# Kernel optimization log

Hardware: AMD Instinct MI355X
Metric: run time of the kernel (lower is better)

Reference implementation:

```python
import jax, jax.numpy as jnp
import numpy as np

DILATIONS = (1, 3, 6, 12)          # layer dilations, flattened from [[1,3],[6,12]]
BLOCKS = ((0, 1), (2, 3))           # block -> layer indices
H_SIZE = 32
STATE_SIZE = 128
OUT_SIZE = STATE_SIZE - H_SIZE      # 96
INPUT_SIZE = 64
OUTPUT_SIZE = 64
T, B = 512, 512


def _linear_params(k, fan_in, fan_out):
    bound = 1.0 / np.sqrt(fan_in)
    kw, kb = jax.random.split(k)
    W = jax.random.uniform(kw, (fan_out, fan_in), minval=-bound, maxval=bound, dtype=jnp.float32)
    b = jax.random.uniform(kb, (fan_out,), minval=-bound, maxval=bound, dtype=jnp.float32)
    return W, b


def setup_inputs() -> dict:
    key = jax.random.key(0)
    ks = jax.random.split(key, 8)
    x = jax.random.normal(ks[0], (T, B, INPUT_SIZE), dtype=jnp.float32)
    ins = [INPUT_SIZE, OUT_SIZE, OUT_SIZE, OUT_SIZE]  # first layer sees raw input
    out = {"x": x}
    for l in range(4):
        W, b = _linear_params(ks[1 + l], ins[l] + 2 * H_SIZE, 4 * STATE_SIZE)
        out[f"W{l}"] = W
        out[f"b{l}"] = b
    Wa, ba = _linear_params(ks[5], OUT_SIZE, OUTPUT_SIZE)
    out["Wa"] = Wa
    out["ba"] = ba
    return out


def _s2cell(W, b, inp, prev_h, second_h, prev_c, delayed_c, has_prev, has_del):
    # xh = cat(input, prev_h, delayed_h-or-prev_h) ; zeros when no prev state (handled by caller masks)
    xh = jnp.concatenate([inp, prev_h, second_h], axis=1)
    g = xh @ W.T + b                                     # [B, 4*state]
    g0, g1, g2, g3 = jnp.split(g, 4, axis=1)
    forget = jax.nn.sigmoid(g0 + 1.0)
    cand = jnp.tanh(g1)
    alpha = jax.nn.sigmoid(g2)
    out_gate = jax.nn.sigmoid(g3)
    weighted = jnp.where(has_del, alpha * prev_c + (1.0 - alpha) * delayed_c, prev_c)
    new_c = jnp.where(has_prev, forget * weighted + (1.0 - forget) * cand, cand)
    whole = out_gate * new_c
    return whole[:, :OUT_SIZE], whole[:, OUT_SIZE:], new_c


def reference(x, W0, b0, W1, b1, W2, b2, W3, b3, Wa, ba):
    Ws = [W0, W1, W2, W3]
    bs = [b0, b1, b2, b3]
    batch = x.shape[1]
    h0 = tuple(jnp.zeros((d, batch, H_SIZE), jnp.float32) for d in DILATIONS)
    c0 = tuple(jnp.zeros((d, batch, STATE_SIZE), jnp.float32) for d in DILATIONS)

    def step(carry, inp_t):
        t, h_bufs, c_bufs = carry
        h_bufs = list(h_bufs)
        c_bufs = list(c_bufs)
        has_prev = t >= 1
        prev_block = None
        out_t = None
        for iblock, layers in enumerate(BLOCKS):
            for j, l in enumerate(layers):
                cur_in = (inp_t if iblock == 0 else prev_block) if j == 0 else out_t
                d = DILATIONS[l]
                # ring buffer: slot (t-1)%d holds state at t-1, slot t%d still holds state at t-d
                prev_h = jnp.where(has_prev, h_bufs[l][(t - 1) % d], 0.0)
                prev_c = c_bufs[l][(t - 1) % d]
                has_del = t >= d
                del_h = jnp.where(has_del, h_bufs[l][t % d], prev_h)
                del_c = c_bufs[l][t % d]
                out_t, new_h, new_c = _s2cell(Ws[l], bs[l], cur_in, prev_h, del_h,
                                              prev_c, del_c, has_prev, has_del)
                h_bufs[l] = h_bufs[l].at[t % d].set(new_h)
                c_bufs[l] = c_bufs[l].at[t % d].set(new_c)
            prev_block = out_t if iblock == 0 else out_t + prev_block  # resnet shortcut
        y = prev_block @ Wa.T + ba
        return (t + 1, tuple(h_bufs), tuple(c_bufs)), y

    _, ys = jax.lax.scan(step, (jnp.int32(0), h0, c0), x)
    return ys  # [T, B, output_size]
```

## Files before the change

### kernel.cpp

```cpp
#include <hip/hip_runtime.h>

typedef unsigned int uint;
typedef unsigned short ushort;
typedef unsigned long long u64;
typedef __attribute__((ext_vector_type(8))) short bf16x8;
typedef __attribute__((ext_vector_type(4))) float f32x4;

#define T_STEPS 512
#define BATCH   512
#define NB      8
#define XS      168
#define CSTR    12
#define OUTC    96
#define FSTR    32

__device__ __forceinline__ ushort f2bf(float f){
  uint u = __builtin_bit_cast(uint, f);
  u = (u + 0x7FFFu + ((u >> 16) & 1u)) >> 16;
  return (ushort)u;
}
__device__ __forceinline__ float bf2f(ushort h){
  uint u = ((uint)h) << 16; return __builtin_bit_cast(float, u);
}
__device__ __forceinline__ float sigm(float x){
  float e = __builtin_exp2f(-1.44269504f * x);
  return __builtin_amdgcn_rcpf(1.0f + e);
}
__device__ __forceinline__ float tanh_fast(float x){
  float e = __builtin_exp2f(-2.88539008f * x);
  return 2.0f * __builtin_amdgcn_rcpf(1.0f + e) - 1.0f;
}
__device__ __forceinline__ uint aload32(const uint* p){
  return __hip_atomic_load(p, __ATOMIC_RELAXED, __HIP_MEMORY_SCOPE_AGENT);
}
__device__ __forceinline__ void astore32(uint* p, uint v){
  __hip_atomic_store(p, v, __ATOMIC_RELAXED, __HIP_MEMORY_SCOPE_AGENT);
}
__device__ __forceinline__ u64 aload64(const u64* p){
  return __hip_atomic_load(p, __ATOMIC_RELAXED, __HIP_MEMORY_SCOPE_AGENT);
}
__device__ __forceinline__ void astore64(u64* p, u64 v){
  __hip_atomic_store(p, v, __ATOMIC_RELAXED, __HIP_MEMORY_SCOPE_AGENT);
}

__global__ __launch_bounds__(512, 1)
void rnn_pipeline(const float* __restrict__ x,
                  const float* __restrict__ W0, const float* __restrict__ b0,
                  const float* __restrict__ W1, const float* __restrict__ b1,
                  const float* __restrict__ W2, const float* __restrict__ b2,
                  const float* __restrict__ W3, const float* __restrict__ b3,
                  const float* __restrict__ Wa, const float* __restrict__ ba,
                  float* __restrict__ y_out,
                  uint* __restrict__ prod, uint* __restrict__ consA,
                  uint* __restrict__ consB,
                  u64* __restrict__ hop0, u64* __restrict__ hop1,
                  u64* __restrict__ hop2, int rd)
{
  const int tid  = threadIdx.x;
  const int wv   = tid >> 6;
  const int lane = tid & 63;
  const int l15  = lane & 15;
  const int hi   = lane >> 4;
  const int rep  = blockIdx.x & 63;
  const int stage= blockIdx.x >> 6;
  const int b0r  = rep * NB;
  const int rmask= rd - 1;

  const int dil = (stage==0)?1:(stage==1)?3:(stage==2)?6:12;
  const int KIN = (stage==0)?64:96;
  const int K   = KIN + 64;
  const float* Wl = (stage==0)?W0:(stage==1)?W1:(stage==2)?W2:W3;
  const float* bl = (stage==0)?b0:(stage==1)?b1:(stage==2)?b2:b3;

  __shared__ __align__(16) ushort xh_hi[16*XS], xh_lo[16*XS];
  __shared__ __align__(16) float  sh_c[12*128*CSTR];
  __shared__ __align__(16) ushort h_hi[12*NB*32], h_lo[12*NB*32];
  __shared__ __align__(16) ushort outp[2304];
  __shared__ __align__(16) ushort o1p[1536];
  __shared__ __align__(16) float  o3f[NB*OUTC];
  __shared__ __align__(16) float  yst[512];

  for (int i = tid; i < 16*XS; i += 512){ xh_hi[i] = 0; xh_lo[i] = 0; }
  for (int i = tid; i < 12*128*CSTR; i += 512) sh_c[i] = 0.0f;
  for (int i = tid; i < 12*NB*32; i += 512){ h_hi[i] = 0; h_lo[i] = 0; }
  for (int i = tid; i < 2304; i += 512) outp[i] = 0;
  for (int i = tid; i < 1536; i += 512) o1p[i] = 0;
  for (int i = tid; i < NB*OUTC; i += 512) o3f[i] = 0.0f;
  yst[tid] = 0.0f;

  const int sidx = 16*wv + l15;

  bf16x8 whi[4][5], wlo[4][5];
  #pragma unroll
  for (int j = 0; j < 4; ++j){
    const int grow = 128*j + sidx;
    #pragma unroll
    for (int ks = 0; ks < 5; ++ks){
      bf16x8 vh, vl;
      const int cb = ks*32 + hi*8;
      if (cb < K){
        const float* p = Wl + (size_t)grow*K + cb;
        #pragma unroll
        for (int i = 0; i < 8; ++i){
          float w = p[i];
          ushort h = f2bf(w);
          vh[i] = (short)h;
          vl[i] = (short)f2bf(w - bf2f(h));
        }
      } else {
        #pragma unroll
        for (int i = 0; i < 8; ++i){ vh[i] = 0; vl[i] = 0; }
      }
      whi[j][ks] = vh; wlo[j][ks] = vl;
    }
  }
  float bias[4];
  #pragma unroll
  for (int j = 0; j < 4; ++j) bias[j] = bl[128*j + sidx];

  bf16x8 phi[3], plo[3];
  #pragma unroll
  for (int ks = 0; ks < 3; ++ks){
    bf16x8 z;
    #pragma unroll
    for (int i = 0; i < 8; ++i) z[i]=0;
    phi[ks]=z; plo[ks]=z;
  }
  float bav = 0.0f;
  if (stage == 3 && wv < 4){
    const int ocol = 16*wv + l15;
    #pragma unroll
    for (int ks = 0; ks < 3; ++ks){
      const float* p = Wa + (size_t)ocol*96 + ks*32 + hi*8;
      bf16x8 vh, vl;
      #pragma unroll
      for (int i = 0; i < 8; ++i){
        float w = p[i];
        ushort h = f2bf(w);
        vh[i] = (short)h;
        vl[i] = (short)f2bf(w - bf2f(h));
      }
      phi[ks] = vh; plo[ks] = vl;
    }
    bav = ba[ocol];
  }

  uint* up_prod  = (stage==1)? &prod[rep*FSTR] : (stage==2)? &prod[(64+rep)*FSTR] :
                   (stage==3)? &prod[(128+rep)*FSTR] : nullptr;
  uint* up_prod1 = (stage==3)? &prod[(64+rep)*FSTR] : nullptr;
  uint* my_prod  = (stage==0)? &prod[rep*FSTR] : (stage==1)? &prod[(64+rep)*FSTR] :
                   (stage==2)? &prod[(128+rep)*FSTR] : nullptr;
  uint* my_consA = (stage==1)? &consA[rep*FSTR] : (stage==2)? &consA[(64+rep)*FSTR] :
                   (stage==3)? &consA[(128+rep)*FSTR] : nullptr;
  uint* my_consB = (stage==3)? &consB[rep*FSTR] : nullptr;
  uint* dnA      = (stage==0)? &consA[rep*FSTR] : (stage==1)? &consA[(64+rep)*FSTR] :
                   (stage==2)? &consA[(128+rep)*FSTR] : nullptr;
  uint* dnB      = (stage==1)? &consB[rep*FSTR] : nullptr;
  const u64* hop_in  = (stage==1)? hop0 : (stage==2)? hop1 : nullptr;
  u64*       hop_out = (stage==0)? hop0 : (stage==1)? hop1 : (stage==2)? hop2 : nullptr;

  __syncthreads();

  u64 pfA = 0, pfB = 0; float xv = 0.0f;
  uint fvU = 0, fvU1 = 0, fvDA = 0, fvDB = 0;
  if (stage == 0){
    xv = x[(size_t)(b0r + (tid>>6))*64 + (tid&63)];
  } else if (stage < 3){
    uint f = aload32(up_prod);
    while (f < 1u){ __builtin_amdgcn_s_sleep(2); f = aload32(up_prod); }
    if (tid < 384) pfA = aload64(hop_in + (size_t)rep*384 + tid);
  } else {
    uint f = aload32(up_prod);
    while (f < 1u){ __builtin_amdgcn_s_sleep(2); f = aload32(up_prod); }
    f = aload32(up_prod1);
    while (f < 1u){ __builtin_amdgcn_s_sleep(2); f = aload32(up_prod1); }
    const u64* s2 = hop2 + (size_t)rep*384;
    const u64* s1 = hop1 + (size_t)rep*384;
    pfA = (tid < 384) ? aload64(s2 + tid) : aload64(s1 + (tid - 384));
    if (tid < 256) pfB = aload64(s1 + 128 + tid);
  }

  int cur = 0, prv = dil - 1;
  for (int t = 0; t < T_STEPS; ++t){
    const int slot = t & rmask;

    asm volatile("s_waitcnt vmcnt(0)" ::: "memory");
    if (stage == 0){
      const int r = tid >> 6, c = tid & 63;
      ushort hb = f2bf(xv);
      xh_hi[r*XS + c] = hb;
      xh_lo[r*XS + c] = f2bf(xv - bf2f(hb));
    } else {
      if (tid < 384){
        const int q = (tid < 192) ? tid : tid - 192;
        ushort* plane = (tid < 192) ? xh_hi : xh_lo;
        const int r = q / 24, c4 = (q % 24) * 4;
        *(u64*)(plane + r*XS + c4) = pfA;
      } else if (stage == 3){
        *(u64*)(o1p + 4*(tid - 384)) = pfA;
      }
      if (stage == 3 && tid < 256) *(u64*)(o1p + 4*(128 + tid)) = pfB;
    }
    {
      const int which = tid >> 8, rem = tid & 255, r = rem >> 5, c = rem & 31;
      const int srcslot = (which == 1 && t >= dil) ? cur : prv;
      xh_hi[r*XS + KIN + which*32 + c] = h_hi[srcslot*(NB*32) + r*32 + c];
      xh_lo[r*XS + KIN + which*32 + c] = h_lo[srcslot*(NB*32) + r*32 + c];
    }
    __syncthreads();
    if (tid == 0){
      if (stage > 0){
        astore32(my_consA, (uint)(t+1));
        if (stage == 3) astore32(my_consB, (uint)(t+1));
      }
      if (stage < 3 && t >= 1) astore32(my_prod, (uint)t);
    }
    if (stage == 3 && t > 0){
      y_out[(size_t)((t-1)*BATCH + b0r + (tid>>6))*64 + (tid&63)] = yst[tid];
    }
    const bool pre = (t + 1 < T_STEPS);
    uint up_f = 0, up_f1 = 0;
    if (pre && stage > 0)  up_f  = aload32(up_prod);
    if (pre && stage == 3) up_f1 = aload32(up_prod1);
    if (stage < 3 && t >= rd)  fvDA = aload32(dnA);
    if (stage == 1 && t >= rd) fvDB = aload32(dnB);

    f32x4 acc[4];
    #pragma unroll
    for (int j = 0; j < 4; ++j) acc[j] = (f32x4){bias[j],bias[j],bias[j],bias[j]};
    const int abase = l15*XS + hi*8;
    #pragma unroll
    for (int ks = 0; ks < 5; ++ks){
      if (ks*32 < K){
        bf16x8 ahi = *(const bf16x8*)(xh_hi + abase + ks*32);
        bf16x8 alo = *(const bf16x8*)(xh_lo + abase + ks*32);
        #pragma unroll
        for (int j = 0; j < 4; ++j){
          acc[j] = __builtin_amdgcn_mfma_f32_16x16x32_bf16(ahi, whi[j][ks], acc[j], 0, 0, 0);
          acc[j] = __builtin_amdgcn_mfma_f32_16x16x32_bf16(alo, whi[j][ks], acc[j], 0, 0, 0);
          acc[j] = __builtin_amdgcn_mfma_f32_16x16x32_bf16(ahi, wlo[j][ks], acc[j], 0, 0, 0);
        }
      }
    }

    if (pre){
      if (stage == 0){
        xv = x[(size_t)((t+1)*BATCH + b0r + (tid>>6))*64 + (tid&63)];
      } else {
        const uint need = (uint)(t + 2);
        while (up_f < need){ __builtin_amdgcn_s_sleep(2); up_f = aload32(up_prod); }
        if (stage == 3)
          while (up_f1 < need){ __builtin_amdgcn_s_sleep(2); up_f1 = aload32(up_prod1); }
        const int ns = (t + 1) & rmask;
        if (stage < 3){
          if (tid < 384) pfA = aload64(hop_in + (size_t)(ns*64 + rep)*384 + tid);
        } else {
          const u64* s2 = hop2 + (size_t)(ns*64 + rep)*384;
          const u64* s1 = hop1 + (size_t)(ns*64 + rep)*384;
          pfA = (tid < 384) ? aload64(s2 + tid) : aload64(s1 + (tid - 384));
          if (tid < 256) pfB = aload64(s1 + 128 + tid);
        }
      }
    }

    f32x4 pc = *(const f32x4*)(sh_c + prv*(128*CSTR) + sidx*CSTR + (hi&1)*4);
    f32x4 dc = *(const f32x4*)(sh_c + cur*(128*CSTR) + sidx*CSTR + (hi&1)*4);
    const bool has_prev = (t >= 1), has_del = (t >= dil);
    f32x4 ncv; float whv[4];
    #pragma unroll
    for (int k = 0; k < 4; ++k){
      float f  = sigm(acc[0][k] + 1.0f);
      float cd = tanh_fast(acc[1][k]);
      float al = sigm(acc[2][k]);
      float og = sigm(acc[3][k]);
      float wt = has_del ? (al*pc[k] + (1.0f - al)*dc[k]) : pc[k];
      float nc = has_prev ? (f*wt + (1.0f - f)*cd) : cd;
      ncv[k] = nc;
      whv[k] = og * nc;
    }
    if (hi < 2){
      *(f32x4*)(sh_c + cur*(128*CSTR) + sidx*CSTR + hi*4) = ncv;
      #pragma unroll
      for (int k = 0; k < 4; ++k){
        const int r = hi*4 + k;
        const float w = whv[k];
        if (sidx < OUTC){
          if (stage == 3){
            o3f[r*OUTC + sidx] = w;
          } else {
            ushort hb = f2bf(w);
            outp[r*OUTC + sidx]       = hb;
            outp[768 + r*OUTC + sidx] = f2bf(w - bf2f(hb));
          }
        } else {
          ushort hb = f2bf(w);
          h_hi[cur*(NB*32) + r*32 + (sidx - OUTC)] = hb;
          h_lo[cur*(NB*32) + r*32 + (sidx - OUTC)] = f2bf(w - bf2f(hb));
        }
      }
    }
    __syncthreads();

    if (stage < 3){
      if (t >= rd){
        const uint need = (uint)(t - rd + 1);
        while (fvDA < need){ __builtin_amdgcn_s_sleep(2); fvDA = aload32(dnA); }
        if (stage == 1)
          while (fvDB < need){ __builtin_amdgcn_s_sleep(2); fvDB = aload32(dnB); }
      }
      if (tid < 384){
        u64 v = *(const u64*)(outp + 4*tid);
        astore64(hop_out + (size_t)(slot*64 + rep)*384 + tid, v);
      }
    } else {
      for (int j = tid; j < 768; j += 512){
        float v = o3f[j] + bf2f(o1p[j]) + bf2f(o1p[768 + j]);
        ushort hb = f2bf(v);
        outp[j]       = hb;
        outp[768 + j] = f2bf(v - bf2f(hb));
      }
      __syncthreads();
      if (wv < 4){
        f32x4 acc1 = (f32x4){bav, bav, bav, bav};
        const int pbase = l15*96 + hi*8;
        #pragma unroll
        for (int ks = 0; ks < 3; ++ks){
          bf16x8 ahi = *(const bf16x8*)(outp + pbase + ks*32);
          bf16x8 alo = *(const bf16x8*)(outp + 768 + pbase + ks*32);
          acc1 = __builtin_amdgcn_mfma_f32_16x16x32_bf16(ahi, phi[ks], acc1, 0, 0, 0);
          acc1 = __builtin_amdgcn_mfma_f32_16x16x32_bf16(alo, phi[ks], acc1, 0, 0, 0);
          acc1 = __builtin_amdgcn_mfma_f32_16x16x32_bf16(ahi, plo[ks], acc1, 0, 0, 0);
        }
        if (hi < 2){
          const int ocol = 16*wv + l15;
          #pragma unroll
          for (int k = 0; k < 4; ++k){
            yst[(hi*4 + k)*64 + ocol] = acc1[k];
          }
        }
      }
    }
    prv = cur;
    cur = (cur + 1 == dil) ? 0 : cur + 1;
  }

  asm volatile("s_waitcnt vmcnt(0)" ::: "memory");
  __syncthreads();
  if (stage == 3){
    y_out[(size_t)((T_STEPS-1)*BATCH + b0r + (tid>>6))*64 + (tid&63)] = yst[tid];
  }
  if (stage < 3 && tid == 0) astore32(my_prod, (uint)(T_STEPS + 2));
}

extern "C" void kernel_launch(void* const* d_in, const int* in_sizes, int n_in,
                              void* d_out, int out_size, void* d_ws, size_t ws_size,
                              hipStream_t stream) {
  (void)in_sizes; (void)n_in; (void)out_size;
  const float* x  = (const float*)d_in[0];
  const float* W0 = (const float*)d_in[1];
  const float* b0 = (const float*)d_in[2];
  const float* W1 = (const float*)d_in[3];
  const float* b1 = (const float*)d_in[4];
  const float* W2 = (const float*)d_in[5];
  const float* b2 = (const float*)d_in[6];
  const float* W3 = (const float*)d_in[7];
  const float* b3 = (const float*)d_in[8];
  const float* Wa = (const float*)d_in[9];
  const float* ba = (const float*)d_in[10];
  float* out = (float*)d_out;

  int rd = 16;
  if (ws_size > 65536){
    size_t avail = ws_size - 65536;
    while (rd < 512 && (size_t)(rd * 2) * 64 * 9216 <= avail) rd *= 2;
  }

  uint* prod  = (uint*)d_ws;
  uint* consA = (uint*)((char*)d_ws + 24576);
  uint* consB = (uint*)((char*)d_ws + 49152);
  u64* hop0 = (u64*)((char*)d_ws + 65536);
  u64* hop1 = hop0 + (size_t)rd*64*384;
  u64* hop2 = hop1 + (size_t)rd*64*384;

  hipMemsetAsync(d_ws, 0, 65536, stream);
  hipLaunchKernelGGL(rnn_pipeline, dim3(256), dim3(512), 0, stream,
                     x, W0, b0, W1, b1, W2, b2, W3, b3, Wa, ba,
                     out, prod, consA, consB, hop0, hop1, hop2, rd);
}
```

Measured before the change: 2.205 ms.

## Process two timesteps per iteration with double-buffered inter-stage handoff

Restructures the persistent pipelined recurrent kernel so each loop iteration handles two timesteps, with double-buffered shared input, output and residual buffers. The h/delayed-h operands are now read directly from a padded h ring buffer instead of being copied into the xh staging array. Flag polling is speculative, falling back to a lane-0 spin and refetch only when the prefetched flags are stale, and producer/consumer signals advance two steps at a time. The final projection is written straight to global memory. The goal is to halve barrier and handshake overhead per step and remove a copy, at the cost of more LDS, a doubled flag protocol whose correctness is subtle, and coarser inter-stage granularity.

```diff
diff --git a/kernel.cpp b/kernel.cpp
--- a/kernel.cpp
+++ b/kernel.cpp
@@ -9,10 +9,13 @@
 #define T_STEPS 512
 #define BATCH   512
 #define NB      8
-#define XS      168
+#define XS      104
+#define HS      40
+#define HSLOT   (16*HS)
 #define CSTR    12
 #define OUTC    96
 #define FSTR    32
+#define NITER   256
 
 __device__ __forceinline__ ushort f2bf(float f){
   uint u = __builtin_bit_cast(uint, f);
@@ -72,21 +75,20 @@
   const float* Wl = (stage==0)?W0:(stage==1)?W1:(stage==2)?W2:W3;
   const float* bl = (stage==0)?b0:(stage==1)?b1:(stage==2)?b2:b3;
 
-  __shared__ __align__(16) ushort xh_hi[16*XS], xh_lo[16*XS];
+  __shared__ __align__(16) ushort xiA_hi[16*XS], xiA_lo[16*XS];
+  __shared__ __align__(16) ushort xiB_hi[16*XS], xiB_lo[16*XS];
   __shared__ __align__(16) float  sh_c[12*128*CSTR];
-  __shared__ __align__(16) ushort h_hi[12*NB*32], h_lo[12*NB*32];
-  __shared__ __align__(16) ushort outp[2304];
-  __shared__ __align__(16) ushort o1p[1536];
-  __shared__ __align__(16) float  o3f[NB*OUTC];
-  __shared__ __align__(16) float  yst[512];
-
-  for (int i = tid; i < 16*XS; i += 512){ xh_hi[i] = 0; xh_lo[i] = 0; }
+  __shared__ __align__(16) ushort h_hi[12*HSLOT], h_lo[12*HSLOT];
+  __shared__ __align__(16) ushort outpA[2304], outpB[2304];
+  __shared__ __align__(16) ushort o1pA[1536], o1pB[1536];
+  __shared__ __align__(16) float  o3fA[768],  o3fB[768];
+
+  for (int i = tid; i < 16*XS; i += 512){ xiA_hi[i]=0; xiA_lo[i]=0; xiB_hi[i]=0; xiB_lo[i]=0; }
   for (int i = tid; i < 12*128*CSTR; i += 512) sh_c[i] = 0.0f;
-  for (int i = tid; i < 12*NB*32; i += 512){ h_hi[i] = 0; h_lo[i] = 0; }
-  for (int i = tid; i < 2304; i += 512) outp[i] = 0;
-  for (int i = tid; i < 1536; i += 512) o1p[i] = 0;
-  for (int i = tid; i < NB*OUTC; i += 512) o3f[i] = 0.0f;
-  yst[tid] = 0.0f;
+  for (int i = tid; i < 12*HSLOT; i += 512){ h_hi[i]=0; h_lo[i]=0; }
+  for (int i = tid; i < 2304; i += 512){ outpA[i]=0; outpB[i]=0; }
+  for (int i = tid; i < 1536; i += 512){ o1pA[i]=0; o1pB[i]=0; }
+  for (int i = tid; i < 768; i += 512){ o3fA[i]=0.0f; o3fB[i]=0.0f; }
 
   const int sidx = 16*wv + l15;
 
@@ -101,15 +103,15 @@
       if (cb < K){
         const float* p = Wl + (size_t)grow*K + cb;
         #pragma unroll
-        for (int i = 0; i < 8; ++i){
-          float w = p[i];
+        for (int q = 0; q < 8; ++q){
+          float w = p[q];
           ushort h = f2bf(w);
-          vh[i] = (short)h;
-          vl[i] = (short)f2bf(w - bf2f(h));
+          vh[q] = (short)h;
+          vl[q] = (short)f2bf(w - bf2f(h));
         }
       } else {
         #pragma unroll
-        for (int i = 0; i < 8; ++i){ vh[i] = 0; vl[i] = 0; }
+        for (int q = 0; q < 8; ++q){ vh[q] = 0; vl[q] = 0; }
       }
       whi[j][ks] = vh; wlo[j][ks] = vl;
     }
@@ -123,7 +125,7 @@
   for (int ks = 0; ks < 3; ++ks){
     bf16x8 z;
     #pragma unroll
-    for (int i = 0; i < 8; ++i) z[i]=0;
+    for (int q = 0; q < 8; ++q) z[q]=0;
     phi[ks]=z; plo[ks]=z;
   }
   float bav = 0.0f;
@@ -134,11 +136,11 @@
       const float* p = Wa + (size_t)ocol*96 + ks*32 + hi*8;
       bf16x8 vh, vl;
       #pragma unroll
-      for (int i = 0; i < 8; ++i){
-        float w = p[i];
+      for (int q = 0; q < 8; ++q){
+        float w = p[q];
         ushort h = f2bf(w);
-        vh[i] = (short)h;
-        vl[i] = (short)f2bf(w - bf2f(h));
+        vh[q] = (short)h;
+        vl[q] = (short)f2bf(w - bf2f(h));
       }
       phi[ks] = vh; plo[ks] = vl;
     }
@@ -159,114 +161,34 @@
   const u64* hop_in  = (stage==1)? hop0 : (stage==2)? hop1 : nullptr;
   u64*       hop_out = (stage==0)? hop0 : (stage==1)? hop1 : (stage==2)? hop2 : nullptr;
 
-  __syncthreads();
-
-  u64 pfA = 0, pfB = 0; float xv = 0.0f;
-  uint fvU = 0, fvU1 = 0, fvDA = 0, fvDB = 0;
-  if (stage == 0){
-    xv = x[(size_t)(b0r + (tid>>6))*64 + (tid&63)];
-  } else if (stage < 3){
-    uint f = aload32(up_prod);
-    while (f < 1u){ __builtin_amdgcn_s_sleep(2); f = aload32(up_prod); }
-    if (tid < 384) pfA = aload64(hop_in + (size_t)rep*384 + tid);
-  } else {
-    uint f = aload32(up_prod);
-    while (f < 1u){ __builtin_amdgcn_s_sleep(2); f = aload32(up_prod); }
-    f = aload32(up_prod1);
-    while (f < 1u){ __builtin_amdgcn_s_sleep(2); f = aload32(up_prod1); }
-    const u64* s2 = hop2 + (size_t)rep*384;
-    const u64* s1 = hop1 + (size_t)rep*384;
-    pfA = (tid < 384) ? aload64(s2 + tid) : aload64(s1 + (tid - 384));
-    if (tid < 256) pfB = aload64(s1 + 128 + tid);
-  }
-
-  int cur = 0, prv = dil - 1;
-  for (int t = 0; t < T_STEPS; ++t){
-    const int slot = t & rmask;
-
-    asm volatile("s_waitcnt vmcnt(0)" ::: "memory");
-    if (stage == 0){
-      const int r = tid >> 6, c = tid & 63;
-      ushort hb = f2bf(xv);
-      xh_hi[r*XS + c] = hb;
-      xh_lo[r*XS + c] = f2bf(xv - bf2f(hb));
-    } else {
-      if (tid < 384){
-        const int q = (tid < 192) ? tid : tid - 192;
-        ushort* plane = (tid < 192) ? xh_hi : xh_lo;
-        const int r = q / 24, c4 = (q % 24) * 4;
-        *(u64*)(plane + r*XS + c4) = pfA;
-      } else if (stage == 3){
-        *(u64*)(o1p + 4*(tid - 384)) = pfA;
-      }
-      if (stage == 3 && tid < 256) *(u64*)(o1p + 4*(128 + tid)) = pfB;
-    }
-    {
-      const int which = tid >> 8, rem = tid & 255, r = rem >> 5, c = rem & 31;
-      const int srcslot = (which == 1 && t >= dil) ? cur : prv;
-      xh_hi[r*XS + KIN + which*32 + c] = h_hi[srcslot*(NB*32) + r*32 + c];
-      xh_lo[r*XS + KIN + which*32 + c] = h_lo[srcslot*(NB*32) + r*32 + c];
-    }
-    __syncthreads();
-    if (tid == 0){
-      if (stage > 0){
-        astore32(my_consA, (uint)(t+1));
-        if (stage == 3) astore32(my_consB, (uint)(t+1));
-      }
-      if (stage < 3 && t >= 1) astore32(my_prod, (uint)t);
-    }
-    if (stage == 3 && t > 0){
-      y_out[(size_t)((t-1)*BATCH + b0r + (tid>>6))*64 + (tid&63)] = yst[tid];
-    }
-    const bool pre = (t + 1 < T_STEPS);
-    uint up_f = 0, up_f1 = 0;
-    if (pre && stage > 0)  up_f  = aload32(up_prod);
-    if (pre && stage == 3) up_f1 = aload32(up_prod1);
-    if (stage < 3 && t >= rd)  fvDA = aload32(dnA);
-    if (stage == 1 && t >= rd) fvDB = aload32(dnB);
-
-    f32x4 acc[4];
-    #pragma unroll
-    for (int j = 0; j < 4; ++j) acc[j] = (f32x4){bias[j],bias[j],bias[j],bias[j]};
-    const int abase = l15*XS + hi*8;
+  const int ax = l15*XS + hi*8;
+  const int ah = l15*HS + hi*8;
+  auto gemm = [&](const ushort* xhi, const ushort* xlo, int pslot, int dslot,
+                  f32x4 acc[4]){
     #pragma unroll
     for (int ks = 0; ks < 5; ++ks){
       if (ks*32 < K){
-        bf16x8 ahi = *(const bf16x8*)(xh_hi + abase + ks*32);
-        bf16x8 alo = *(const bf16x8*)(xh_lo + abase + ks*32);
+        const ushort *ph, *pl; int off;
+        if (ks*32 < KIN){ ph = xhi; pl = xlo; off = ax + ks*32; }
+        else if (ks*32 == KIN){ ph = h_hi; pl = h_lo; off = pslot*HSLOT + ah; }
+        else { ph = h_hi; pl = h_lo; off = dslot*HSLOT + ah; }
+        bf16x8 a_hi = *(const bf16x8*)(ph + off);
+        bf16x8 a_lo = *(const bf16x8*)(pl + off);
         #pragma unroll
         for (int j = 0; j < 4; ++j){
-          acc[j] = __builtin_amdgcn_mfma_f32_16x16x32_bf16(ahi, whi[j][ks], acc[j], 0, 0, 0);
-          acc[j] = __builtin_amdgcn_mfma_f32_16x16x32_bf16(alo, whi[j][ks], acc[j], 0, 0, 0);
-          acc[j] = __builtin_amdgcn_mfma_f32_16x16x32_bf16(ahi, wlo[j][ks], acc[j], 0, 0, 0);
-        }
-      }
-    }
-
-    if (pre){
-      if (stage == 0){
-        xv = x[(size_t)((t+1)*BATCH + b0r + (tid>>6))*64 + (tid&63)];
-      } else {
-        const uint need = (uint)(t + 2);
-        while (up_f < need){ __builtin_amdgcn_s_sleep(2); up_f = aload32(up_prod); }
-        if (stage == 3)
-          while (up_f1 < need){ __builtin_amdgcn_s_sleep(2); up_f1 = aload32(up_prod1); }
-        const int ns = (t + 1) & rmask;
-        if (stage < 3){
-          if (tid < 384) pfA = aload64(hop_in + (size_t)(ns*64 + rep)*384 + tid);
-        } else {
-          const u64* s2 = hop2 + (size_t)(ns*64 + rep)*384;
-          const u64* s1 = hop1 + (size_t)(ns*64 + rep)*384;
-          pfA = (tid < 384) ? aload64(s2 + tid) : aload64(s1 + (tid - 384));
-          if (tid < 256) pfB = aload64(s1 + 128 + tid);
-        }
-      }
-    }
-
-    f32x4 pc = *(const f32x4*)(sh_c + prv*(128*CSTR) + sidx*CSTR + (hi&1)*4);
-    f32x4 dc = *(const f32x4*)(sh_c + cur*(128*CSTR) + sidx*CSTR + (hi&1)*4);
-    const bool has_prev = (t >= 1), has_del = (t >= dil);
-    f32x4 ncv; float whv[4];
+          acc[j] = __builtin_amdgcn_mfma_f32_16x16x32_bf16(a_hi, whi[j][ks], acc[j], 0, 0, 0);
+          acc[j] = __builtin_amdgcn_mfma_f32_16x16x32_bf16(a_lo, whi[j][ks], acc[j], 0, 0, 0);
+          acc[j] = __builtin_amdgcn_mfma_f32_16x16x32_bf16(a_hi, wlo[j][ks], acc[j], 0, 0, 0);
+        }
+      }
+    }
+  };
+  auto gates = [&](const f32x4 acc[4], f32x4 pc, int cslot, bool has_prev,
+                   bool has_del, ushort* outp, float* o3, f32x4& ncv_out){
+    f32x4 dc;
+    if (dil == 1) dc = pc;
+    else dc = *(const f32x4*)(sh_c + cslot*(128*CSTR) + sidx*CSTR + (hi&1)*4);
+    float whv[4];
     #pragma unroll
     for (int k = 0; k < 4; ++k){
       float f  = sigm(acc[0][k] + 1.0f);
@@ -275,18 +197,18 @@
       float og = sigm(acc[3][k]);
       float wt = has_del ? (al*pc[k] + (1.0f - al)*dc[k]) : pc[k];
       float nc = has_prev ? (f*wt + (1.0f - f)*cd) : cd;
-      ncv[k] = nc;
+      ncv_out[k] = nc;
       whv[k] = og * nc;
     }
     if (hi < 2){
-      *(f32x4*)(sh_c + cur*(128*CSTR) + sidx*CSTR + hi*4) = ncv;
+      *(f32x4*)(sh_c + cslot*(128*CSTR) + sidx*CSTR + hi*4) = ncv_out;
       #pragma unroll
       for (int k = 0; k < 4; ++k){
         const int r = hi*4 + k;
         const float w = whv[k];
         if (sidx < OUTC){
           if (stage == 3){
-            o3f[r*OUTC + sidx] = w;
+            o3[r*OUTC + sidx] = w;
           } else {
             ushort hb = f2bf(w);
             outp[r*OUTC + sidx]       = hb;
@@ -294,62 +216,198 @@
           }
         } else {
           ushort hb = f2bf(w);
-          h_hi[cur*(NB*32) + r*32 + (sidx - OUTC)] = hb;
-          h_lo[cur*(NB*32) + r*32 + (sidx - OUTC)] = f2bf(w - bf2f(hb));
+          h_hi[cslot*HSLOT + r*HS + (sidx - OUTC)] = hb;
+          h_lo[cslot*HSLOT + r*HS + (sidx - OUTC)] = f2bf(w - bf2f(hb));
+        }
+      }
+    }
+  };
+  auto proj = [&](const ushort* outp, int s){
+    if (wv < 4){
+      f32x4 a1 = (f32x4){bav, bav, bav, bav};
+      const int pbase = l15*96 + hi*8;
+      #pragma unroll
+      for (int ks = 0; ks < 3; ++ks){
+        bf16x8 a_hi = *(const bf16x8*)(outp + pbase + ks*32);
+        bf16x8 a_lo = *(const bf16x8*)(outp + 768 + pbase + ks*32);
+        a1 = __builtin_amdgcn_mfma_f32_16x16x32_bf16(a_hi, phi[ks], a1, 0, 0, 0);
+        a1 = __builtin_amdgcn_mfma_f32_16x16x32_bf16(a_lo, phi[ks], a1, 0, 0, 0);
+        a1 = __builtin_amdgcn_mfma_f32_16x16x32_bf16(a_hi, plo[ks], a1, 0, 0, 0);
+      }
+      if (hi < 2){
+        const int ocol = 16*wv + l15;
+        #pragma unroll
+        for (int k = 0; k < 4; ++k)
+          y_out[(size_t)(s*BATCH + b0r + hi*4 + k)*64 + ocol] = a1[k];
+      }
+    }
+  };
+
+  __syncthreads();
+
+  u64 pfA_t = 0, pfA_u = 0, pfC_t = 0, pfC_u = 0;
+  float xv_t = 0.0f, xv_u = 0.0f;
+  uint fvU = 0, fvU1 = 0, fvDA = 0, fvDB = 0;
+  if (stage == 0){
+    xv_t = x[(size_t)(b0r + (tid>>6))*64 + (tid&63)];
+    xv_u = x[(size_t)(BATCH + b0r + (tid>>6))*64 + (tid&63)];
+  } else if (stage < 3){
+    do { fvU = aload32(up_prod); if (fvU < 4u) __builtin_amdgcn_s_sleep(2); } while (fvU < 4u);
+    if (tid < 384){
+      pfA_t = aload64(hop_in + (size_t)rep*384 + tid);
+      pfA_u = aload64(hop_in + (size_t)(64 + rep)*384 + tid);
+    }
+  } else {
+    do { fvU  = aload32(up_prod);  if (fvU  < 4u) __builtin_amdgcn_s_sleep(2); } while (fvU  < 4u);
+    do { fvU1 = aload32(up_prod1); if (fvU1 < 4u) __builtin_amdgcn_s_sleep(2); } while (fvU1 < 4u);
+    if (tid < 384){
+      pfA_t = aload64(hop2 + (size_t)rep*384 + tid);
+      pfA_u = aload64(hop2 + (size_t)(64 + rep)*384 + tid);
+      pfC_t = aload64(hop1 + (size_t)rep*384 + tid);
+      pfC_u = aload64(hop1 + (size_t)(64 + rep)*384 + tid);
+    }
+  }
+
+  f32x4 ncv_prev = (f32x4){0.0f, 0.0f, 0.0f, 0.0f};
+  int cur_t = 0, prv_t = dil - 1;
+
+  for (int it = 0; it < NITER; ++it){
+    const int t = 2*it, u = t + 1;
+    const int slot_t = t & rmask, slot_u = u & rmask;
+    const int cur_u = (cur_t + 1 == dil) ? 0 : cur_t + 1;
+    const int del_t = (t >= dil) ? cur_t : prv_t;
+    const int del_u = (u >= dil) ? cur_u : cur_t;
+
+    if (stage > 0){
+      const bool bad = (fvU < (uint)(t+4)) || (stage == 3 && fvU1 < (uint)(t+4));
+      if (bad){
+        if (lane == 0){
+          while (aload32(up_prod) < (uint)(t+2)) __builtin_amdgcn_s_sleep(2);
+          if (stage == 3)
+            while (aload32(up_prod1) < (uint)(t+2)) __builtin_amdgcn_s_sleep(2);
+        }
+        if (tid < 384){
+          if (stage < 3){
+            pfA_t = aload64(hop_in + (size_t)(slot_t*64 + rep)*384 + tid);
+            pfA_u = aload64(hop_in + (size_t)(slot_u*64 + rep)*384 + tid);
+          } else {
+            pfA_t = aload64(hop2 + (size_t)(slot_t*64 + rep)*384 + tid);
+            pfA_u = aload64(hop2 + (size_t)(slot_u*64 + rep)*384 + tid);
+            pfC_t = aload64(hop1 + (size_t)(slot_t*64 + rep)*384 + tid);
+            pfC_u = aload64(hop1 + (size_t)(slot_u*64 + rep)*384 + tid);
+          }
+        }
+      }
+    }
+    if (stage == 0){
+      const int r = tid >> 6, c = tid & 63;
+      ushort hb = f2bf(xv_t);
+      xiA_hi[r*XS + c] = hb; xiA_lo[r*XS + c] = f2bf(xv_t - bf2f(hb));
+      hb = f2bf(xv_u);
+      xiB_hi[r*XS + c] = hb; xiB_lo[r*XS + c] = f2bf(xv_u - bf2f(hb));
+    } else {
+      if (tid < 384){
+        const int q = (tid < 192) ? tid : tid - 192;
+        const int off = (q/24)*XS + (q%24)*4;
+        ushort* plA = (tid < 192) ? xiA_hi : xiA_lo;
+        ushort* plB = (tid < 192) ? xiB_hi : xiB_lo;
+        *(u64*)(plA + off) = pfA_t;
+        *(u64*)(plB + off) = pfA_u;
+        if (stage == 3){
+          *(u64*)(o1pA + 4*tid) = pfC_t;
+          *(u64*)(o1pB + 4*tid) = pfC_u;
         }
       }
     }
     __syncthreads();
+    if (tid == 0){
+      if (stage > 0){
+        astore32(my_consA, (uint)(t+2));
+        if (stage == 3) astore32(my_consB, (uint)(t+2));
+      }
+      if (stage < 3 && it >= 2) astore32(my_prod, (uint)(t-2));
+    }
+    if (stage < 3 && u >= rd){
+      const bool badc = (fvDA < (uint)(t+4-rd)) || (stage == 1 && fvDB < (uint)(t+4-rd));
+      if (badc && lane == 0){
+        while (aload32(dnA) < (uint)(t+2-rd)) __builtin_amdgcn_s_sleep(2);
+        if (stage == 1)
+          while (aload32(dnB) < (uint)(t+2-rd)) __builtin_amdgcn_s_sleep(2);
+      }
+    }
+    if (it + 1 < NITER){
+      const int nt = (t+2) & rmask, nu = (t+3) & rmask;
+      if (stage == 0){
+        xv_t = x[(size_t)((t+2)*BATCH + b0r + (tid>>6))*64 + (tid&63)];
+        xv_u = x[(size_t)((t+3)*BATCH + b0r + (tid>>6))*64 + (tid&63)];
+      } else if (stage < 3){
+        if (tid < 384){
+          pfA_t = aload64(hop_in + (size_t)(nt*64 + rep)*384 + tid);
+          pfA_u = aload64(hop_in + (size_t)(nu*64 + rep)*384 + tid);
+        }
+        fvU = aload32(up_prod);
+      } else {
+        if (tid < 384){
+          pfA_t = aload64(hop2 + (size_t)(nt*64 + rep)*384 + tid);
+          pfA_u = aload64(hop2 + (size_t)(nu*64 + rep)*384 + tid);
+          pfC_t = aload64(hop1 + (size_t)(nt*64 + rep)*384 + tid);
+          pfC_u = aload64(hop1 + (size_t)(nu*64 + rep)*384 + tid);
+        }
+        fvU  = aload32(up_prod);
+        fvU1 = aload32(up_prod1);
+      }
+    }
+    if (stage < 3) fvDA = aload32(dnA);
+    if (stage == 1) fvDB = aload32(dnB);
+    asm volatile("" ::: "memory");
+
+    f32x4 acc[4];
+    #pragma unroll
+    for (int j = 0; j < 4; ++j) acc[j] = (f32x4){bias[j],bias[j],bias[j],bias[j]};
+    gemm(xiA_hi, xiA_lo, prv_t, del_t, acc);
+    f32x4 ncv;
+    gates(acc, ncv_prev, cur_t, (t >= 1), (t >= dil), outpA, o3fA, ncv);
+    ncv_prev = ncv;
+    __syncthreads();
+
+    if (stage == 3){
+      for (int j = tid; j < 768; j += 512){
+        float v = o3fA[j] + bf2f(o1pA[j]) + bf2f(o1pA[768 + j]);
+        ushort hb = f2bf(v);
+        outpA[j]       = hb;
+        outpA[768 + j] = f2bf(v - bf2f(hb));
+      }
+    }
+    #pragma unroll
+    for (int j = 0; j < 4; ++j) acc[j] = (f32x4){bias[j],bias[j],bias[j],bias[j]};
+    gemm(xiB_hi, xiB_lo, cur_t, del_u, acc);
+    gates(acc, ncv_prev, cur_u, true, (u >= dil), outpB, o3fB, ncv);
+    ncv_prev = ncv;
+    __syncthreads();
 
     if (stage < 3){
-      if (t >= rd){
-        const uint need = (uint)(t - rd + 1);
-        while (fvDA < need){ __builtin_amdgcn_s_sleep(2); fvDA = aload32(dnA); }
-        if (stage == 1)
-          while (fvDB < need){ __builtin_amdgcn_s_sleep(2); fvDB = aload32(dnB); }
-      }
       if (tid < 384){
-        u64 v = *(const u64*)(outp + 4*tid);
-        astore64(hop_out + (size_t)(slot*64 + rep)*384 + tid, v);
+        astore64(hop_out + (size_t)(slot_t*64 + rep)*384 + tid, *(const u64*)(outpA + 4*tid));
+        astore64(hop_out + (size_t)(slot_u*64 + rep)*384 + tid, *(const u64*)(outpB + 4*tid));
       }
     } else {
+      proj(outpA, t);
       for (int j = tid; j < 768; j += 512){
-        float v = o3f[j] + bf2f(o1p[j]) + bf2f(o1p[768 + j]);
+        float v = o3fB[j] + bf2f(o1pB[j]) + bf2f(o1pB[768 + j]);
         ushort hb = f2bf(v);
-        outp[j]       = hb;
-        outp[768 + j] = f2bf(v - bf2f(hb));
+        outpB[j]       = hb;
+        outpB[768 + j] = f2bf(v - bf2f(hb));
       }
       __syncthreads();
-      if (wv < 4){
-        f32x4 acc1 = (f32x4){bav, bav, bav, bav};
-        const int pbase = l15*96 + hi*8;
-        #pragma unroll
-        for (int ks = 0; ks < 3; ++ks){
-          bf16x8 ahi = *(const bf16x8*)(outp + pbase + ks*32);
-          bf16x8 alo = *(const bf16x8*)(outp + 768 + pbase + ks*32);
-          acc1 = __builtin_amdgcn_mfma_f32_16x16x32_bf16(ahi, phi[ks], acc1, 0, 0, 0);
-          acc1 = __builtin_amdgcn_mfma_f32_16x16x32_bf16(alo, phi[ks], acc1, 0, 0, 0);
-          acc1 = __builtin_amdgcn_mfma_f32_16x16x32_bf16(ahi, plo[ks], acc1, 0, 0, 0);
-        }
-        if (hi < 2){
-          const int ocol = 16*wv + l15;
-          #pragma unroll
-          for (int k = 0; k < 4; ++k){
-            yst[(hi*4 + k)*64 + ocol] = acc1[k];
-          }
-        }
-      }
-    }
-    prv = cur;
-    cur = (cur + 1 == dil) ? 0 : cur + 1;
+      proj(outpB, u);
+    }
+    prv_t = cur_u;
+    cur_t = (cur_u + 1 == dil) ? 0 : cur_u + 1;
   }
 
   asm volatile("s_waitcnt vmcnt(0)" ::: "memory");
   __syncthreads();
-  if (stage == 3){
-    y_out[(size_t)((T_STEPS-1)*BATCH + b0r + (tid>>6))*64 + (tid&63)] = yst[tid];
-  }
-  if (stage < 3 && tid == 0) astore32(my_prod, (uint)(T_STEPS + 2));
+  if (stage < 3 && tid == 0) astore32(my_prod, (uint)(T_STEPS + 8));
 }
 
 extern "C" void kernel_launch(void* const* d_in, const int* in_sizes, int n_in,
```

Result: faster. 2.095 ms (-5.0%).
